# Optimization experiments

Hardware: AMD Instinct MI355X
Metric: run time of the kernel (lower is better)

The kernel has to match this reference:

```python
import jax, jax.numpy as jnp
import numpy as np

N = 26000       # total nodes (1040 graphs * 25 joints)
E = 208000      # total edges
G = 1040        # graphs (16 samples * 65 frames)
FRAMES = 65
F_IN = 6
HID = 128
HEADS = 4
NCLS = 7


def setup_inputs() -> dict:
    key = jax.random.key(0)
    ks = jax.random.split(key, 30)

    def nrm(k, shape, s=0.05):
        return jax.random.normal(k, shape, dtype=jnp.float32) * s

    return {
        "x": jax.random.normal(ks[0], (N, F_IN), dtype=jnp.float32),
        "edge_index": jax.random.randint(ks[1], (2, E), 0, N, dtype=jnp.int32),
        "batch": jnp.arange(N, dtype=jnp.int32) // (N // G),  # 25 nodes per graph
        "w1_root": nrm(ks[2], (F_IN, HID)),
        "w1_nei": nrm(ks[3], (F_IN, HID)),
        "b1": nrm(ks[4], (HID,)),
        "wq": nrm(ks[5], (HID, HEADS * HID)),
        "bq": nrm(ks[6], (HEADS * HID,)),
        "wk": nrm(ks[7], (HID, HEADS * HID)),
        "bk": nrm(ks[8], (HEADS * HID,)),
        "wv": nrm(ks[9], (HID, HEADS * HID)),
        "bv": nrm(ks[10], (HEADS * HID,)),
        "wskip": nrm(ks[11], (HID, HEADS * HID)),
        "bskip": nrm(ks[12], (HEADS * HID,)),
        "skip_w": nrm(ks[13], (HID, HEADS * HID)),
        "lin1_w": nrm(ks[14], (HEADS * HID, HID)),
        "lin1_b": nrm(ks[15], (HID,)),
        "l2_root": nrm(ks[16], (HID, HID)),
        "l2_nei": nrm(ks[17], (HID, HID)),
        "l2_b": nrm(ks[18], (HID,)),
        "l3_root": nrm(ks[19], (HID, HID)),
        "l3_nei": nrm(ks[20], (HID, HID)),
        "l3_b": nrm(ks[21], (HID,)),
        "fc_w": nrm(ks[22], (HID, NCLS)),
        "fc_b": nrm(ks[23], (NCLS,)),
    }


def _graph_conv(x, src, dst, w_root, w_nei, b):
    # PyG GraphConv (aggr='add'): W_root x_i + W_nei * sum_{j in N(i)} x_j + b
    agg = jax.ops.segment_sum(x[src], dst, num_segments=N)
    return x @ w_root + agg @ w_nei + b


def _transformer_conv(x, src, dst, wq, bq, wk, bk, wv, bv, wskip, bskip):
    # PyG TransformerConv, concat=True, root_weight=True, beta=False.
    # Dropout on attention is inference-disabled.
    q = (x @ wq + bq).reshape(N, HEADS, HID)
    k = (x @ wk + bk).reshape(N, HEADS, HID)
    v = (x @ wv + bv).reshape(N, HEADS, HID)
    logits = jnp.einsum('ehc,ehc->eh', q[dst], k[src]) / jnp.sqrt(jnp.float32(HID))
    m = jax.ops.segment_max(logits, dst, num_segments=N)          # [N,H]
    a = jnp.exp(logits - m[dst])                                  # [E,H]
    denom = jax.ops.segment_sum(a, dst, num_segments=N)           # [N,H]
    num = jax.ops.segment_sum(a[:, :, None] * v[src], dst, num_segments=N)  # [N,H,C]
    out = num / jnp.where(denom == 0, 1.0, denom)[:, :, None]
    return out.reshape(N, HEADS * HID) + (x @ wskip + bskip)


def reference(x, edge_index, batch,
              w1_root, w1_nei, b1,
              wq, bq, wk, bk, wv, bv, wskip, bskip,
              skip_w, lin1_w, lin1_b,
              l2_root, l2_nei, l2_b,
              l3_root, l3_nei, l3_b,
              fc_w, fc_b):
    src, dst = edge_index[0], edge_index[1]
    h = jax.nn.relu(_graph_conv(x, src, dst, w1_root, w1_nei, b1))
    skip_out = h @ skip_w  # external skip Linear (no bias)
    h = jax.nn.relu(_transformer_conv(h, src, dst, wq, bq, wk, bk, wv, bv, wskip, bskip) + skip_out)
    h = jax.nn.relu(h @ lin1_w + lin1_b)
    for wr, wn, b in ((l2_root, l2_nei, l2_b), (l3_root, l3_nei, l3_b)):
        h = jax.nn.relu(_graph_conv(h, src, dst, wr, wn, b) + h)
    # global_mean_pool over graphs
    sums = jax.ops.segment_sum(h, batch, num_segments=G)
    cnts = jax.ops.segment_sum(jnp.ones((N,), jnp.float32), batch, num_segments=G)
    pooled = sums / jnp.where(cnts == 0, 1.0, cnts)[:, None]      # [G, HID]
    # average over 65 frames per sample, then classify
    z = pooled.reshape(-1, FRAMES, HID).mean(axis=1)              # [G/65, HID]
    return z @ fc_w + fc_b
```

## Files before the change

kernel.cpp:

```cpp
#include <hip/hip_runtime.h>
#include <math.h>

#define NN 26000
#define NE 208000
#define SCAN_CH 26

typedef __attribute__((ext_vector_type(8))) short bf16x8;
typedef __attribute__((ext_vector_type(4))) float f32x4;
typedef __attribute__((ext_vector_type(2))) float f32x2;
typedef unsigned char u8;

__device__ __forceinline__ float bf2f(ushort u){
  union { unsigned int i; float f; } w; w.i = ((unsigned int)u) << 16; return w.f;
}
__device__ __forceinline__ ushort f2bf(float f){
  union { float f; unsigned int i; } w; w.f = f;
  unsigned int u = w.i + 0x7fffu + ((w.i >> 16) & 1u);
  return (ushort)(u >> 16);
}

__global__ void count_k(const int* __restrict__ dst, int* __restrict__ cnt, int E){
  int e = blockIdx.x*256 + threadIdx.x;
  if (e < E) atomicAdd(&cnt[dst[e]], 1);
}

__global__ __launch_bounds__(1024) void scan_k(int* __restrict__ cnt_cur, int* __restrict__ off){
  int t = threadIdx.x;
  int base = t * SCAN_CH;
  int v[SCAN_CH];
  #pragma unroll
  for (int j = 0; j < SCAN_CH; ++j){
    int idx = base + j;
    v[j] = (idx < NN) ? cnt_cur[idx] : 0;
  }
  int s = 0;
  #pragma unroll
  for (int j = 0; j < SCAN_CH; ++j) s += v[j];
  __shared__ int ls[1024];
  ls[t] = s; __syncthreads();
  for (int ofs = 1; ofs < 1024; ofs <<= 1){
    int u = (t >= ofs) ? ls[t - ofs] : 0;
    __syncthreads();
    ls[t] += u;
    __syncthreads();
  }
  int run = (t == 0) ? 0 : ls[t-1];
  #pragma unroll
  for (int j = 0; j < SCAN_CH; ++j){
    int idx = base + j;
    if (idx < NN){
      off[idx] = run;
      cnt_cur[idx] = run;
      run += v[j];
    }
  }
  if (t == 1023) off[NN] = ls[1023];
}

__global__ void fill_k(const int* __restrict__ src, const int* __restrict__ dst,
                       int* __restrict__ cur, int* __restrict__ csrc, int E){
  int e = blockIdx.x*256 + threadIdx.x;
  if (e < E){
    int p = atomicAdd(&cur[dst[e]], 1);
    csrc[p] = src[e];
  }
}

__global__ __launch_bounds__(256) void layer1_k(
    const float* __restrict__ x, const int* __restrict__ off,
    const int* __restrict__ csrc, const float* __restrict__ w1r,
    const float* __restrict__ w1n, const float* __restrict__ b1,
    ushort* __restrict__ h1)
{
  __shared__ float aggs[2][6];
  int slot = threadIdx.x >> 7, c = threadIdx.x & 127;
  int i = blockIdx.x*2 + slot;
  if (c < 6){
    float s = 0.f;
    int e1 = off[i+1];
    for (int j = off[i]; j < e1; ++j) s += x[(size_t)csrc[j]*6 + c];
    aggs[slot][c] = s;
  }
  __syncthreads();
  float s = b1[c];
  #pragma unroll
  for (int f = 0; f < 6; ++f){
    s = fmaf(x[i*6+f],    w1r[f*128+c], s);
    s = fmaf(aggs[slot][f], w1n[f*128+c], s);
  }
  h1[(size_t)i*128 + c] = f2bf(fmaxf(s, 0.f));
}

__global__ void prep_w(const float* __restrict__ wq, const float* __restrict__ wk,
                       const float* __restrict__ wv, const float* __restrict__ wskip,
                       const float* __restrict__ skw, const float* __restrict__ lin1w,
                       const float* __restrict__ l2r, const float* __restrict__ l2n,
                       const float* __restrict__ l3r, const float* __restrict__ l3n,
                       ushort* __restrict__ wbuf){
  int idx = blockIdx.x*256 + threadIdx.x;
  if (idx >= 393216) return;
  float v;
  if (idx < 262144){
    int seg = idx >> 16;
    int local = idx & 65535;
    int n = local >> 7, kk = local & 127;
    const float* w = (seg == 0) ? wq : (seg == 1) ? wk : (seg == 2) ? wv : wskip;
    v = w[kk*512 + n];
    if (seg == 3) v += skw[kk*512 + n];
  } else if (idx < 327680){
    int local = idx - 262144;
    int n = local >> 9, kk = local & 511;
    v = lin1w[kk*128 + n];
  } else {
    int rem = idx - 327680;
    int seg = rem >> 14;
    int local = rem & 16383;
    int n = local >> 7, kk = local & 127;
    const float* w = (seg == 0) ? l2r : (seg == 1) ? l2n : (seg == 2) ? l3r : l3n;
    v = w[kk*128 + n];
  }
  wbuf[idx] = f2bf(v);
}

__global__ __launch_bounds__(256) void qkvs_k(
    const ushort* __restrict__ A, const ushort* __restrict__ BT,
    const float* __restrict__ bq, const float* __restrict__ bk,
    const float* __restrict__ bv, const float* __restrict__ bs,
    u8* __restrict__ cq, u8* __restrict__ ckv,
    ushort* __restrict__ cs, int M)
{
  __shared__ ushort As[128][72];
  int tid  = threadIdx.x;
  int lane = tid & 63;
  int wid  = tid >> 6;
  int wr = wid >> 1, wc = wid & 1;
  int rowbase = blockIdx.y * 128;
  int seg = blockIdx.x >> 2;
  const float* bias = (seg == 0) ? bq : (seg == 1) ? bk : (seg == 2) ? bv : bs;
  int colloc = (blockIdx.x & 3) * 128;
  int lr = lane & 15, lk = (lane >> 4) * 8;

  f32x4 acc[4][4] = {};

  #pragma unroll
  for (int k0 = 0; k0 < 128; k0 += 64){
    __syncthreads();
    #pragma unroll
    for (int i = 0; i < 4; ++i){
      int c = tid + i*256;
      int r = c >> 3, col8 = (c & 7) * 8;
      int row = rowbase + r;
      bf16x8 av = (bf16x8)0;
      if (row < M) av = *reinterpret_cast<const bf16x8*>(A + (size_t)row*128 + k0 + col8);
      *reinterpret_cast<bf16x8*>(&As[r][col8]) = av;
    }
    __syncthreads();
    #pragma unroll
    for (int ks = 0; ks < 64; ks += 32){
      bf16x8 af[4], bfr[4];
      #pragma unroll
      for (int i = 0; i < 4; ++i)
        af[i] = *reinterpret_cast<const bf16x8*>(&As[wr*64 + i*16 + lr][ks + lk]);
      #pragma unroll
      for (int j = 0; j < 4; ++j)
        bfr[j] = *reinterpret_cast<const bf16x8*>(
            BT + (size_t)(blockIdx.x*128 + wc*64 + j*16 + lr)*128 + k0 + ks + lk);
      #pragma unroll
      for (int i = 0; i < 4; ++i)
        #pragma unroll
        for (int j = 0; j < 4; ++j)
          acc[i][j] = __builtin_amdgcn_mfma_f32_16x16x32_bf16(af[i], bfr[j], acc[i][j], 0, 0, 0);
    }
  }

  int rq = lane >> 4;
  if (seg <= 2){
    u8* tile = (u8*)&As[0][0];
    __syncthreads();
    #pragma unroll
    for (int i = 0; i < 4; ++i)
      #pragma unroll
      for (int r = 0; r < 4; ++r){
        int lrow = wr*64 + i*16 + rq*4 + r;
        #pragma unroll
        for (int j = 0; j < 4; ++j){
          int lcol = wc*64 + j*16 + lr;
          float v = acc[i][j][r] + bias[colloc + lcol];
          unsigned int pk = __builtin_amdgcn_cvt_pk_fp8_f32(v, v, 0u, false);
          tile[lrow*136 + lcol] = (u8)(pk & 0xffu);
        }
      }
    __syncthreads();
    u8* Cb; int ldb, cb;
    if (seg == 0){ Cb = cq;  ldb = 512;  cb = colloc; }
    else         { Cb = ckv; ldb = 1024; cb = (seg == 1 ? 0 : 512) + colloc; }
    #pragma unroll
    for (int t = tid; t < 2048; t += 256){
      int r = t >> 4, b8 = (t & 15) * 8;
      int row = rowbase + r;
      if (row < M)
        *reinterpret_cast<uint2*>(Cb + (size_t)row*ldb + cb + b8) =
            *reinterpret_cast<const uint2*>(&tile[r*136 + b8]);
    }
  } else {
    ushort* tile = &As[0][0];
    #pragma unroll
    for (int p = 0; p < 2; ++p){
      __syncthreads();
      if (wr == p){
        #pragma unroll
        for (int i = 0; i < 4; ++i)
          #pragma unroll
          for (int r = 0; r < 4; ++r){
            int lrow = i*16 + rq*4 + r;
            #pragma unroll
            for (int j = 0; j < 4; ++j){
              int lcol = wc*64 + j*16 + lr;
              tile[lrow*136 + lcol] = f2bf(acc[i][j][r] + bias[colloc + lcol]);
            }
          }
      }
      __syncthreads();
      #pragma unroll
      for (int t = tid; t < 1024; t += 256){
        int r = t >> 4, s8 = (t & 15) * 8;
        int row = rowbase + p*64 + r;
        if (row < M)
          *reinterpret_cast<bf16x8*>(cs + (size_t)row*512 + colloc + s8) =
              *reinterpret_cast<const bf16x8*>(&tile[r*136 + s8]);
      }
    }
  }
}

__global__ __launch_bounds__(256) void bgemm64_k(
    const ushort* __restrict__ A1, int lda1, const ushort* __restrict__ B1T, int K1,
    const float* __restrict__ bias, ushort* __restrict__ C, int M, int N)
{
  __shared__ ushort As[64][72];
  int tid  = threadIdx.x;
  int lane = tid & 63;
  int wid  = tid >> 6;
  int wr = wid >> 1, wc = wid & 1;
  int rowbase = blockIdx.y * 64;
  int colbase = blockIdx.x * 128;
  int lr = lane & 15, lk = (lane >> 4) * 8;

  f32x4 acc[2][4] = {};

  for (int k0 = 0; k0 < K1; k0 += 64){
    __syncthreads();
    #pragma unroll
    for (int i = 0; i < 2; ++i){
      int c = tid + i*256;
      int r = c >> 3, col8 = (c & 7) * 8;
      int row = rowbase + r;
      bf16x8 av = (bf16x8)0;
      if (row < M) av = *reinterpret_cast<const bf16x8*>(A1 + (size_t)row*lda1 + k0 + col8);
      *reinterpret_cast<bf16x8*>(&As[r][col8]) = av;
    }
    __syncthreads();
    #pragma unroll
    for (int ks = 0; ks < 64; ks += 32){
      bf16x8 af[2], bfr[4];
      #pragma unroll
      for (int i = 0; i < 2; ++i)
        af[i] = *reinterpret_cast<const bf16x8*>(&As[wr*32 + i*16 + lr][ks + lk]);
      #pragma unroll
      for (int j = 0; j < 4; ++j)
        bfr[j] = *reinterpret_cast<const bf16x8*>(
            B1T + (size_t)(colbase + wc*64 + j*16 + lr)*K1 + k0 + ks + lk);
      #pragma unroll
      for (int i = 0; i < 2; ++i)
        #pragma unroll
        for (int j = 0; j < 4; ++j)
          acc[i][j] = __builtin_amdgcn_mfma_f32_16x16x32_bf16(af[i], bfr[j], acc[i][j], 0, 0, 0);
    }
  }

  int rq = lane >> 4;
  #pragma unroll
  for (int i = 0; i < 2; ++i){
    #pragma unroll
    for (int r = 0; r < 4; ++r){
      int row = rowbase + wr*32 + i*16 + rq*4 + r;
      if (row >= M) continue;
      #pragma unroll
      for (int j = 0; j < 4; ++j){
        int col = colbase + wc*64 + j*16 + lr;
        if (col >= N) continue;
        float v = fmaxf(acc[i][j][r] + bias[col], 0.f);
        C[(size_t)row*N + col] = f2bf(v);
      }
    }
  }
}

__global__ __launch_bounds__(256) void gconv_k(
    const ushort* __restrict__ h, const ushort* __restrict__ WrT,
    const ushort* __restrict__ WnT, const float* __restrict__ bias,
    const int* __restrict__ off, const int* __restrict__ csrc,
    ushort* __restrict__ out, int M)
{
  __shared__ ushort As1[64][136];
  __shared__ ushort As2[64][136];
  int tid = threadIdx.x, lane = tid & 63, wid = tid >> 6;
  int wr = wid >> 1, wc = wid & 1;
  int rowbase = blockIdx.x * 64;
  int lr = lane & 15, lk = (lane >> 4) * 8;

  #pragma unroll
  for (int it = 0; it < 4; ++it){
    int c = tid + it*256;
    int r = c >> 4, col8 = (c & 15) * 8;
    int row = rowbase + r;
    bf16x8 av = (bf16x8)0;
    if (row < M) av = *reinterpret_cast<const bf16x8*>(h + (size_t)row*128 + col8);
    *reinterpret_cast<bf16x8*>(&As1[r][col8]) = av;
  }
  {
    int r = tid >> 2, sl = tid & 3;
    int row = rowbase + r;
    float a[32] = {};
    if (row < M){
      int e1 = off[row+1];
      for (int j = off[row]; j < e1; ++j){
        const ushort* hp = h + (size_t)csrc[j]*128 + sl*32;
        #pragma unroll
        for (int u = 0; u < 4; ++u){
          bf16x8 hv = *reinterpret_cast<const bf16x8*>(hp + u*8);
          #pragma unroll
          for (int p = 0; p < 8; ++p) a[u*8+p] += bf2f((ushort)hv[p]);
        }
      }
    }
    #pragma unroll
    for (int u = 0; u < 4; ++u){
      bf16x8 o;
      #pragma unroll
      for (int p = 0; p < 8; ++p) o[p] = (short)f2bf(a[u*8+p]);
      *reinterpret_cast<bf16x8*>(&As2[r][sl*32 + u*8]) = o;
    }
  }
  __syncthreads();

  f32x4 acc[2][4] = {};
  #pragma unroll
  for (int pass = 0; pass < 2; ++pass){
    const ushort* BT = pass ? WnT : WrT;
    #pragma unroll
    for (int kk = 0; kk < 128; kk += 32){
      bf16x8 af[2], bfr[4];
      #pragma unroll
      for (int i = 0; i < 2; ++i)
        af[i] = pass
          ? *reinterpret_cast<const bf16x8*>(&As2[wr*32 + i*16 + lr][kk + lk])
          : *reinterpret_cast<const bf16x8*>(&As1[wr*32 + i*16 + lr][kk + lk]);
      #pragma unroll
      for (int j = 0; j < 4; ++j)
        bfr[j] = *reinterpret_cast<const bf16x8*>(
            BT + (size_t)(wc*64 + j*16 + lr)*128 + kk + lk);
      #pragma unroll
      for (int i = 0; i < 2; ++i)
        #pragma unroll
        for (int j = 0; j < 4; ++j)
          acc[i][j] = __builtin_amdgcn_mfma_f32_16x16x32_bf16(af[i], bfr[j], acc[i][j], 0, 0, 0);
    }
  }

  int rq = lane >> 4;
  #pragma unroll
  for (int i = 0; i < 2; ++i){
    #pragma unroll
    for (int r = 0; r < 4; ++r){
      int lrow = wr*32 + i*16 + rq*4 + r;
      int row = rowbase + lrow;
      if (row >= M) continue;
      #pragma unroll
      for (int j = 0; j < 4; ++j){
        int col = wc*64 + j*16 + lr;
        float v = acc[i][j][r] + bias[col] + bf2f(As1[lrow][col]);
        out[(size_t)row*128 + col] = f2bf(fmaxf(v, 0.f));
      }
    }
  }
}

__global__ __launch_bounds__(256) void attn_k(
    const u8* __restrict__ q, const u8* __restrict__ kv,
    ushort* __restrict__ s_io,
    const int* __restrict__ off, const int* __restrict__ csrc)
{
  int lane = threadIdx.x & 63;
  int i = blockIdx.x*4 + (threadIdx.x >> 6);
  uint2 qv = *reinterpret_cast<const uint2*>(q + (size_t)i*512 + lane*8);
  f32x2 q01 = __builtin_amdgcn_cvt_pk_f32_fp8(qv.x, false);
  f32x2 q23 = __builtin_amdgcn_cvt_pk_f32_fp8(qv.x, true);
  f32x2 q45 = __builtin_amdgcn_cvt_pk_f32_fp8(qv.y, false);
  f32x2 q67 = __builtin_amdgcn_cvt_pk_f32_fp8(qv.y, true);
  float qf[8] = {q01[0], q01[1], q23[0], q23[1], q45[0], q45[1], q67[0], q67[1]};

  float d = 0.f, acc[8] = {};
  int e0 = off[i], e1 = off[i+1];
  uint2 kA, vA, kB, vB;
  if (e0 < e1){
    const u8* r = kv + (size_t)csrc[e0]*1024 + lane*8;
    kA = *reinterpret_cast<const uint2*>(r);
    vA = *reinterpret_cast<const uint2*>(r + 512);
  }
  if (e0 + 1 < e1){
    const u8* r = kv + (size_t)csrc[e0+1]*1024 + lane*8;
    kB = *reinterpret_cast<const uint2*>(r);
    vB = *reinterpret_cast<const uint2*>(r + 512);
  }
  for (int j = e0; j < e1; ++j){
    uint2 kc = kA, vc = vA;
    kA = kB; vA = vB;
    if (j + 2 < e1){
      const u8* r = kv + (size_t)csrc[j+2]*1024 + lane*8;
      kB = *reinterpret_cast<const uint2*>(r);
      vB = *reinterpret_cast<const uint2*>(r + 512);
    }
    f32x2 k01 = __builtin_amdgcn_cvt_pk_f32_fp8(kc.x, false);
    f32x2 k23 = __builtin_amdgcn_cvt_pk_f32_fp8(kc.x, true);
    f32x2 k45 = __builtin_amdgcn_cvt_pk_f32_fp8(kc.y, false);
    f32x2 k67 = __builtin_amdgcn_cvt_pk_f32_fp8(kc.y, true);
    float t;
    t = qf[0] * k01[0];
    t = fmaf(qf[1], k01[1], t);
    t = fmaf(qf[2], k23[0], t);
    t = fmaf(qf[3], k23[1], t);
    t = fmaf(qf[4], k45[0], t);
    t = fmaf(qf[5], k45[1], t);
    t = fmaf(qf[6], k67[0], t);
    t = fmaf(qf[7], k67[1], t);
    t += __shfl_xor(t, 1);
    t += __shfl_xor(t, 2);
    t += __shfl_xor(t, 4);
    t += __shfl_xor(t, 8);
    float w = __expf(t * 0.08838834764831845f);
    d += w;
    f32x2 v01 = __builtin_amdgcn_cvt_pk_f32_fp8(vc.x, false);
    f32x2 v23 = __builtin_amdgcn_cvt_pk_f32_fp8(vc.x, true);
    f32x2 v45 = __builtin_amdgcn_cvt_pk_f32_fp8(vc.y, false);
    f32x2 v67 = __builtin_amdgcn_cvt_pk_f32_fp8(vc.y, true);
    acc[0] = fmaf(w, v01[0], acc[0]);
    acc[1] = fmaf(w, v01[1], acc[1]);
    acc[2] = fmaf(w, v23[0], acc[2]);
    acc[3] = fmaf(w, v23[1], acc[3]);
    acc[4] = fmaf(w, v45[0], acc[4]);
    acc[5] = fmaf(w, v45[1], acc[5]);
    acc[6] = fmaf(w, v67[0], acc[6]);
    acc[7] = fmaf(w, v67[1], acc[7]);
  }
  float inv = (d > 0.f) ? 1.f/d : 0.f;
  ushort* rowp = s_io + (size_t)i*512 + lane*8;
  bf16x8 sk8 = *reinterpret_cast<const bf16x8*>(rowp);
  bf16x8 o8;
  #pragma unroll
  for (int p = 0; p < 8; ++p)
    o8[p] = (short)f2bf(fmaxf(bf2f((ushort)sk8[p]) + acc[p]*inv, 0.f));
  *reinterpret_cast<bf16x8*>(rowp) = o8;
}

__global__ __launch_bounds__(256) void fc1_k(const ushort* __restrict__ h,
                                             float* __restrict__ partial){
  int s = blockIdx.x, c0 = blockIdx.y;
  int t = threadIdx.x;
  int c = t & 127, g = t >> 7;
  float sum = 0.f;
  int rend = (c0 + 1) * 125;
  for (int r = c0*125 + g; r < rend; r += 2)
    sum += bf2f(h[((size_t)s*1625 + r)*128 + c]);
  __shared__ float zs[2][128];
  zs[g][c] = sum; __syncthreads();
  if (g == 0) partial[((size_t)s*13 + c0)*128 + c] = zs[0][c] + zs[1][c];
}

__global__ __launch_bounds__(128) void fc2_k(const float* __restrict__ partial,
    const float* __restrict__ fcw, const float* __restrict__ fcb,
    float* __restrict__ out)
{
  int s = blockIdx.x;
  int c = threadIdx.x;
  float z = 0.f;
  #pragma unroll
  for (int p = 0; p < 13; ++p) z += partial[((size_t)s*13 + p)*128 + c];
  __shared__ float zs[128];
  zs[c] = z * (1.0f/1625.0f);
  __syncthreads();
  if (c < 7){
    float o = fcb[c];
    for (int k2 = 0; k2 < 128; ++k2) o = fmaf(zs[k2], fcw[k2*7 + c], o);
    out[s*7 + c] = o;
  }
}

extern "C" void kernel_launch(void* const* d_in, const int* in_sizes, int n_in,
                              void* d_out, int out_size, void* d_ws, size_t ws_size,
                              hipStream_t stream)
{
  const float* x     = (const float*)d_in[0];
  const int*   ei    = (const int*)  d_in[1];
  const float* w1r   = (const float*)d_in[3];
  const float* w1n   = (const float*)d_in[4];
  const float* b1    = (const float*)d_in[5];
  const float* wq    = (const float*)d_in[6];
  const float* bq    = (const float*)d_in[7];
  const float* wk    = (const float*)d_in[8];
  const float* bk    = (const float*)d_in[9];
  const float* wv    = (const float*)d_in[10];
  const float* bv    = (const float*)d_in[11];
  const float* wskip = (const float*)d_in[12];
  const float* bskip = (const float*)d_in[13];
  const float* skw   = (const float*)d_in[14];
  const float* lin1w = (const float*)d_in[15];
  const float* lin1b = (const float*)d_in[16];
  const float* l2r   = (const float*)d_in[17];
  const float* l2n   = (const float*)d_in[18];
  const float* l2b   = (const float*)d_in[19];
  const float* l3r   = (const float*)d_in[20];
  const float* l3n   = (const float*)d_in[21];
  const float* l3b   = (const float*)d_in[22];
  const float* fcw   = (const float*)d_in[23];
  const float* fcb   = (const float*)d_in[24];
  float* out = (float*)d_out;

  const int* src = ei;
  const int* dst = ei + NE;

  char* base = (char*)d_ws;
  size_t o = 0;
  auto alloc = [&](size_t bytes) -> void* {
    o = (o + 255) & ~(size_t)255;
    void* p = base + o; o += bytes; return p;
  };
  int*    cnt     = (int*)   alloc((size_t)NN*4);
  int*    off     = (int*)   alloc((size_t)(NN+1)*4);
  int*    csrc    = (int*)   alloc((size_t)NE*4);
  float*  partial = (float*) alloc((size_t)16*13*128*4);
  ushort* h1      = (ushort*)alloc((size_t)NN*128*2);
  ushort* wbuf    = (ushort*)alloc((size_t)393216*2);
  u8*     bufQ8   = (u8*)    alloc((size_t)NN*512);
  u8*     bufKV   = (u8*)    alloc((size_t)NN*1024);
  ushort* bufS    = (ushort*)alloc((size_t)NN*512*2);
  ushort* hbuf    = (ushort*)alloc((size_t)NN*256*2);
  (void)ws_size; (void)in_sizes; (void)n_in; (void)out_size;

  const ushort* lin1T = wbuf + 262144;
  const ushort* l2rT  = wbuf + 327680;
  const ushort* l2nT  = wbuf + 344064;
  const ushort* l3rT  = wbuf + 360448;
  const ushort* l3nT  = wbuf + 376832;

  ushort* h3 = hbuf;
  ushort* h4 = hbuf + (size_t)NN*128;
  ushort* h5 = bufS;

  hipMemsetAsync(cnt, 0, (size_t)NN*4, stream);
  count_k<<<(NE+255)/256, 256, 0, stream>>>(dst, cnt, NE);
  scan_k<<<1, 1024, 0, stream>>>(cnt, off);
  fill_k<<<(NE+255)/256, 256, 0, stream>>>(src, dst, cnt, csrc, NE);

  layer1_k<<<NN/2, 256, 0, stream>>>(x, off, csrc, w1r, w1n, b1, h1);

  prep_w<<<1536, 256, 0, stream>>>(wq, wk, wv, wskip, skw, lin1w, l2r, l2n, l3r, l3n, wbuf);

  {
    dim3 g(16, (NN+127)/128);
    qkvs_k<<<g, 256, 0, stream>>>(h1, wbuf, bq, bk, bv, bskip,
                                  bufQ8, bufKV, bufS, NN);
  }

  attn_k<<<NN/4, 256, 0, stream>>>(bufQ8, bufKV, bufS, off, csrc);

  {
    dim3 g(1, (NN+63)/64);
    bgemm64_k<<<g, 256, 0, stream>>>(bufS, 512, lin1T, 512, lin1b, h3, NN, 128);
  }

  gconv_k<<<(NN+63)/64, 256, 0, stream>>>(h3, l2rT, l2nT, l2b, off, csrc, h4, NN);
  gconv_k<<<(NN+63)/64, 256, 0, stream>>>(h4, l3rT, l3nT, l3b, off, csrc, h5, NN);

  {
    dim3 g1(16, 13);
    fc1_k<<<g1, 256, 0, stream>>>(h5, partial);
    fc2_k<<<16, 128, 0, stream>>>(partial, fcw, fcb, out);
  }
}
```

Before: 304.6 us.

## Fuse edge count with weight prep, stage B tiles in LDS, merge final FC kernels

Merges the degree-count kernel and the weight-conversion kernel into one launch by splitting blocks by index. The QKVS and bgemm GEMMs now stage the B (weight) tile in shared memory instead of reading it straight from global per fragment. The QKVS epilogue writes bf16 to LDS once and converts to fp8 with packed 4-wide conversions. The two-stage pooling/classifier becomes a single kernel with 16 blocks. That removes launches, but the per-sample reduction of 1625 rows now runs on very few blocks.

```diff
diff --git a/kernel.cpp b/kernel.cpp
--- a/kernel.cpp
+++ b/kernel.cpp
@@ -4,6 +4,7 @@
 #define NN 26000
 #define NE 208000
 #define SCAN_CH 26
+#define CNT_BLOCKS 813
 
 typedef __attribute__((ext_vector_type(8))) short bf16x8;
 typedef __attribute__((ext_vector_type(4))) float f32x4;
@@ -19,85 +20,19 @@
   return (ushort)(u >> 16);
 }
 
-__global__ void count_k(const int* __restrict__ dst, int* __restrict__ cnt, int E){
-  int e = blockIdx.x*256 + threadIdx.x;
-  if (e < E) atomicAdd(&cnt[dst[e]], 1);
-}
-
-__global__ __launch_bounds__(1024) void scan_k(int* __restrict__ cnt_cur, int* __restrict__ off){
-  int t = threadIdx.x;
-  int base = t * SCAN_CH;
-  int v[SCAN_CH];
-  #pragma unroll
-  for (int j = 0; j < SCAN_CH; ++j){
-    int idx = base + j;
-    v[j] = (idx < NN) ? cnt_cur[idx] : 0;
-  }
-  int s = 0;
-  #pragma unroll
-  for (int j = 0; j < SCAN_CH; ++j) s += v[j];
-  __shared__ int ls[1024];
-  ls[t] = s; __syncthreads();
-  for (int ofs = 1; ofs < 1024; ofs <<= 1){
-    int u = (t >= ofs) ? ls[t - ofs] : 0;
-    __syncthreads();
-    ls[t] += u;
-    __syncthreads();
-  }
-  int run = (t == 0) ? 0 : ls[t-1];
-  #pragma unroll
-  for (int j = 0; j < SCAN_CH; ++j){
-    int idx = base + j;
-    if (idx < NN){
-      off[idx] = run;
-      cnt_cur[idx] = run;
-      run += v[j];
-    }
-  }
-  if (t == 1023) off[NN] = ls[1023];
-}
-
-__global__ void fill_k(const int* __restrict__ src, const int* __restrict__ dst,
-                       int* __restrict__ cur, int* __restrict__ csrc, int E){
-  int e = blockIdx.x*256 + threadIdx.x;
-  if (e < E){
-    int p = atomicAdd(&cur[dst[e]], 1);
-    csrc[p] = src[e];
-  }
-}
-
-__global__ __launch_bounds__(256) void layer1_k(
-    const float* __restrict__ x, const int* __restrict__ off,
-    const int* __restrict__ csrc, const float* __restrict__ w1r,
-    const float* __restrict__ w1n, const float* __restrict__ b1,
-    ushort* __restrict__ h1)
-{
-  __shared__ float aggs[2][6];
-  int slot = threadIdx.x >> 7, c = threadIdx.x & 127;
-  int i = blockIdx.x*2 + slot;
-  if (c < 6){
-    float s = 0.f;
-    int e1 = off[i+1];
-    for (int j = off[i]; j < e1; ++j) s += x[(size_t)csrc[j]*6 + c];
-    aggs[slot][c] = s;
-  }
-  __syncthreads();
-  float s = b1[c];
-  #pragma unroll
-  for (int f = 0; f < 6; ++f){
-    s = fmaf(x[i*6+f],    w1r[f*128+c], s);
-    s = fmaf(aggs[slot][f], w1n[f*128+c], s);
-  }
-  h1[(size_t)i*128 + c] = f2bf(fmaxf(s, 0.f));
-}
-
-__global__ void prep_w(const float* __restrict__ wq, const float* __restrict__ wk,
-                       const float* __restrict__ wv, const float* __restrict__ wskip,
-                       const float* __restrict__ skw, const float* __restrict__ lin1w,
-                       const float* __restrict__ l2r, const float* __restrict__ l2n,
-                       const float* __restrict__ l3r, const float* __restrict__ l3n,
-                       ushort* __restrict__ wbuf){
-  int idx = blockIdx.x*256 + threadIdx.x;
+__global__ void cp_k(const int* __restrict__ dst, int* __restrict__ cnt,
+                     const float* __restrict__ wq, const float* __restrict__ wk,
+                     const float* __restrict__ wv, const float* __restrict__ wskip,
+                     const float* __restrict__ skw, const float* __restrict__ lin1w,
+                     const float* __restrict__ l2r, const float* __restrict__ l2n,
+                     const float* __restrict__ l3r, const float* __restrict__ l3n,
+                     ushort* __restrict__ wbuf){
+  if (blockIdx.x < CNT_BLOCKS){
+    int e = blockIdx.x*256 + threadIdx.x;
+    if (e < NE) atomicAdd(&cnt[dst[e]], 1);
+    return;
+  }
+  int idx = (blockIdx.x - CNT_BLOCKS)*256 + threadIdx.x;
   if (idx >= 393216) return;
   float v;
   if (idx < 262144){
@@ -122,6 +57,73 @@
   wbuf[idx] = f2bf(v);
 }
 
+__global__ __launch_bounds__(1024) void scan_k(int* __restrict__ cnt_cur, int* __restrict__ off){
+  int t = threadIdx.x;
+  int base = t * SCAN_CH;
+  int v[SCAN_CH];
+  #pragma unroll
+  for (int j = 0; j < SCAN_CH; ++j){
+    int idx = base + j;
+    v[j] = (idx < NN) ? cnt_cur[idx] : 0;
+  }
+  int s = 0;
+  #pragma unroll
+  for (int j = 0; j < SCAN_CH; ++j) s += v[j];
+  __shared__ int ls[1024];
+  ls[t] = s; __syncthreads();
+  for (int ofs = 1; ofs < 1024; ofs <<= 1){
+    int u = (t >= ofs) ? ls[t - ofs] : 0;
+    __syncthreads();
+    ls[t] += u;
+    __syncthreads();
+  }
+  int run = (t == 0) ? 0 : ls[t-1];
+  #pragma unroll
+  for (int j = 0; j < SCAN_CH; ++j){
+    int idx = base + j;
+    if (idx < NN){
+      off[idx] = run;
+      cnt_cur[idx] = run;
+      run += v[j];
+    }
+  }
+  if (t == 1023) off[NN] = ls[1023];
+}
+
+__global__ void fill_k(const int* __restrict__ src, const int* __restrict__ dst,
+                       int* __restrict__ cur, int* __restrict__ csrc, int E){
+  int e = blockIdx.x*256 + threadIdx.x;
+  if (e < E){
+    int p = atomicAdd(&cur[dst[e]], 1);
+    csrc[p] = src[e];
+  }
+}
+
+__global__ __launch_bounds__(256) void layer1_k(
+    const float* __restrict__ x, const int* __restrict__ off,
+    const int* __restrict__ csrc, const float* __restrict__ w1r,
+    const float* __restrict__ w1n, const float* __restrict__ b1,
+    ushort* __restrict__ h1)
+{
+  __shared__ float aggs[2][6];
+  int slot = threadIdx.x >> 7, c = threadIdx.x & 127;
+  int i = blockIdx.x*2 + slot;
+  if (c < 6){
+    float s = 0.f;
+    int e1 = off[i+1];
+    for (int j = off[i]; j < e1; ++j) s += x[(size_t)csrc[j]*6 + c];
+    aggs[slot][c] = s;
+  }
+  __syncthreads();
+  float s = b1[c];
+  #pragma unroll
+  for (int f = 0; f < 6; ++f){
+    s = fmaf(x[i*6+f],    w1r[f*128+c], s);
+    s = fmaf(aggs[slot][f], w1n[f*128+c], s);
+  }
+  h1[(size_t)i*128 + c] = f2bf(fmaxf(s, 0.f));
+}
+
 __global__ __launch_bounds__(256) void qkvs_k(
     const ushort* __restrict__ A, const ushort* __restrict__ BT,
     const float* __restrict__ bq, const float* __restrict__ bk,
@@ -129,7 +131,9 @@
     u8* __restrict__ cq, u8* __restrict__ ckv,
     ushort* __restrict__ cs, int M)
 {
-  __shared__ ushort As[128][72];
+  __shared__ ushort smem[2*128*72];
+  ushort* Asm = smem;
+  ushort* Bsm = smem + 128*72;
   int tid  = threadIdx.x;
   int lane = tid & 63;
   int wid  = tid >> 6;
@@ -142,9 +146,7 @@
 
   f32x4 acc[4][4] = {};
 
-  #pragma unroll
   for (int k0 = 0; k0 < 128; k0 += 64){
-    __syncthreads();
     #pragma unroll
     for (int i = 0; i < 4; ++i){
       int c = tid + i*256;
@@ -152,7 +154,9 @@
       int row = rowbase + r;
       bf16x8 av = (bf16x8)0;
       if (row < M) av = *reinterpret_cast<const bf16x8*>(A + (size_t)row*128 + k0 + col8);
-      *reinterpret_cast<bf16x8*>(&As[r][col8]) = av;
+      *reinterpret_cast<bf16x8*>(&Asm[r*72 + col8]) = av;
+      *reinterpret_cast<bf16x8*>(&Bsm[r*72 + col8]) =
+          *reinterpret_cast<const bf16x8*>(BT + (size_t)(blockIdx.x*128 + r)*128 + k0 + col8);
     }
     __syncthreads();
     #pragma unroll
@@ -160,75 +164,60 @@
       bf16x8 af[4], bfr[4];
       #pragma unroll
       for (int i = 0; i < 4; ++i)
-        af[i] = *reinterpret_cast<const bf16x8*>(&As[wr*64 + i*16 + lr][ks + lk]);
+        af[i] = *reinterpret_cast<const bf16x8*>(&Asm[(wr*64 + i*16 + lr)*72 + ks + lk]);
       #pragma unroll
       for (int j = 0; j < 4; ++j)
-        bfr[j] = *reinterpret_cast<const bf16x8*>(
-            BT + (size_t)(blockIdx.x*128 + wc*64 + j*16 + lr)*128 + k0 + ks + lk);
+        bfr[j] = *reinterpret_cast<const bf16x8*>(&Bsm[(wc*64 + j*16 + lr)*72 + ks + lk]);
       #pragma unroll
       for (int i = 0; i < 4; ++i)
         #pragma unroll
         for (int j = 0; j < 4; ++j)
           acc[i][j] = __builtin_amdgcn_mfma_f32_16x16x32_bf16(af[i], bfr[j], acc[i][j], 0, 0, 0);
     }
+    __syncthreads();
   }
 
   int rq = lane >> 4;
+  #pragma unroll
+  for (int i = 0; i < 4; ++i)
+    #pragma unroll
+    for (int r = 0; r < 4; ++r){
+      int lrow = wr*64 + i*16 + rq*4 + r;
+      #pragma unroll
+      for (int j = 0; j < 4; ++j){
+        int lcol = wc*64 + j*16 + lr;
+        smem[lrow*136 + lcol] = f2bf(acc[i][j][r] + bias[colloc + lcol]);
+      }
+    }
+  __syncthreads();
+
   if (seg <= 2){
-    u8* tile = (u8*)&As[0][0];
-    __syncthreads();
-    #pragma unroll
-    for (int i = 0; i < 4; ++i)
-      #pragma unroll
-      for (int r = 0; r < 4; ++r){
-        int lrow = wr*64 + i*16 + rq*4 + r;
-        #pragma unroll
-        for (int j = 0; j < 4; ++j){
-          int lcol = wc*64 + j*16 + lr;
-          float v = acc[i][j][r] + bias[colloc + lcol];
-          unsigned int pk = __builtin_amdgcn_cvt_pk_fp8_f32(v, v, 0u, false);
-          tile[lrow*136 + lcol] = (u8)(pk & 0xffu);
-        }
-      }
-    __syncthreads();
     u8* Cb; int ldb, cb;
     if (seg == 0){ Cb = cq;  ldb = 512;  cb = colloc; }
     else         { Cb = ckv; ldb = 1024; cb = (seg == 1 ? 0 : 512) + colloc; }
     #pragma unroll
     for (int t = tid; t < 2048; t += 256){
-      int r = t >> 4, b8 = (t & 15) * 8;
+      int r = t >> 4, s8 = (t & 15) * 8;
+      int row = rowbase + r;
+      if (row < M){
+        bf16x8 hv = *reinterpret_cast<const bf16x8*>(&smem[r*136 + s8]);
+        unsigned int lo = 0, hi = 0;
+        lo = __builtin_amdgcn_cvt_pk_fp8_f32(bf2f((ushort)hv[0]), bf2f((ushort)hv[1]), lo, false);
+        lo = __builtin_amdgcn_cvt_pk_fp8_f32(bf2f((ushort)hv[2]), bf2f((ushort)hv[3]), lo, true);
+        hi = __builtin_amdgcn_cvt_pk_fp8_f32(bf2f((ushort)hv[4]), bf2f((ushort)hv[5]), hi, false);
+        hi = __builtin_amdgcn_cvt_pk_fp8_f32(bf2f((ushort)hv[6]), bf2f((ushort)hv[7]), hi, true);
+        uint2 o; o.x = lo; o.y = hi;
+        *reinterpret_cast<uint2*>(Cb + (size_t)row*ldb + cb + s8) = o;
+      }
+    }
+  } else {
+    #pragma unroll
+    for (int t = tid; t < 2048; t += 256){
+      int r = t >> 4, s8 = (t & 15) * 8;
       int row = rowbase + r;
       if (row < M)
-        *reinterpret_cast<uint2*>(Cb + (size_t)row*ldb + cb + b8) =
-            *reinterpret_cast<const uint2*>(&tile[r*136 + b8]);
-    }
-  } else {
-    ushort* tile = &As[0][0];
-    #pragma unroll
-    for (int p = 0; p < 2; ++p){
-      __syncthreads();
-      if (wr == p){
-        #pragma unroll
-        for (int i = 0; i < 4; ++i)
-          #pragma unroll
-          for (int r = 0; r < 4; ++r){
-            int lrow = i*16 + rq*4 + r;
-            #pragma unroll
-            for (int j = 0; j < 4; ++j){
-              int lcol = wc*64 + j*16 + lr;
-              tile[lrow*136 + lcol] = f2bf(acc[i][j][r] + bias[colloc + lcol]);
-            }
-          }
-      }
-      __syncthreads();
-      #pragma unroll
-      for (int t = tid; t < 1024; t += 256){
-        int r = t >> 4, s8 = (t & 15) * 8;
-        int row = rowbase + p*64 + r;
-        if (row < M)
-          *reinterpret_cast<bf16x8*>(cs + (size_t)row*512 + colloc + s8) =
-              *reinterpret_cast<const bf16x8*>(&tile[r*136 + s8]);
-      }
+        *reinterpret_cast<bf16x8*>(cs + (size_t)row*512 + colloc + s8) =
+            *reinterpret_cast<const bf16x8*>(&smem[r*136 + s8]);
     }
   }
 }
@@ -238,6 +227,7 @@
     const float* __restrict__ bias, ushort* __restrict__ C, int M, int N)
 {
   __shared__ ushort As[64][72];
+  __shared__ ushort Bs[128][72];
   int tid  = threadIdx.x;
   int lane = tid & 63;
   int wid  = tid >> 6;
@@ -249,7 +239,6 @@
   f32x4 acc[2][4] = {};
 
   for (int k0 = 0; k0 < K1; k0 += 64){
-    __syncthreads();
     #pragma unroll
     for (int i = 0; i < 2; ++i){
       int c = tid + i*256;
@@ -259,6 +248,13 @@
       if (row < M) av = *reinterpret_cast<const bf16x8*>(A1 + (size_t)row*lda1 + k0 + col8);
       *reinterpret_cast<bf16x8*>(&As[r][col8]) = av;
     }
+    #pragma unroll
+    for (int i = 0; i < 4; ++i){
+      int c = tid + i*256;
+      int r = c >> 3, col8 = (c & 7) * 8;
+      *reinterpret_cast<bf16x8*>(&Bs[r][col8]) =
+          *reinterpret_cast<const bf16x8*>(B1T + (size_t)(colbase + r)*K1 + k0 + col8);
+    }
     __syncthreads();
     #pragma unroll
     for (int ks = 0; ks < 64; ks += 32){
@@ -268,14 +264,14 @@
         af[i] = *reinterpret_cast<const bf16x8*>(&As[wr*32 + i*16 + lr][ks + lk]);
       #pragma unroll
       for (int j = 0; j < 4; ++j)
-        bfr[j] = *reinterpret_cast<const bf16x8*>(
-            B1T + (size_t)(colbase + wc*64 + j*16 + lr)*K1 + k0 + ks + lk);
+        bfr[j] = *reinterpret_cast<const bf16x8*>(&Bs[wc*64 + j*16 + lr][ks + lk]);
       #pragma unroll
       for (int i = 0; i < 2; ++i)
         #pragma unroll
         for (int j = 0; j < 4; ++j)
           acc[i][j] = __builtin_amdgcn_mfma_f32_16x16x32_bf16(af[i], bfr[j], acc[i][j], 0, 0, 0);
     }
+    __syncthreads();
   }
 
   int rq = lane >> 4;
@@ -463,36 +459,24 @@
   *reinterpret_cast<bf16x8*>(rowp) = o8;
 }
 
-__global__ __launch_bounds__(256) void fc1_k(const ushort* __restrict__ h,
-                                             float* __restrict__ partial){
-  int s = blockIdx.x, c0 = blockIdx.y;
+__global__ __launch_bounds__(256) void fc_k(const ushort* __restrict__ h,
+    const float* __restrict__ fcw, const float* __restrict__ fcb,
+    float* __restrict__ out)
+{
+  int s = blockIdx.x;
   int t = threadIdx.x;
   int c = t & 127, g = t >> 7;
   float sum = 0.f;
-  int rend = (c0 + 1) * 125;
-  for (int r = c0*125 + g; r < rend; r += 2)
+  for (int r = g; r < 1625; r += 2)
     sum += bf2f(h[((size_t)s*1625 + r)*128 + c]);
   __shared__ float zs[2][128];
   zs[g][c] = sum; __syncthreads();
-  if (g == 0) partial[((size_t)s*13 + c0)*128 + c] = zs[0][c] + zs[1][c];
-}
-
-__global__ __launch_bounds__(128) void fc2_k(const float* __restrict__ partial,
-    const float* __restrict__ fcw, const float* __restrict__ fcb,
-    float* __restrict__ out)
-{
-  int s = blockIdx.x;
-  int c = threadIdx.x;
-  float z = 0.f;
-  #pragma unroll
-  for (int p = 0; p < 13; ++p) z += partial[((size_t)s*13 + p)*128 + c];
-  __shared__ float zs[128];
-  zs[c] = z * (1.0f/1625.0f);
+  if (t < 128) zs[0][t] = (zs[0][t] + zs[1][t]) * (1.0f/1625.0f);
   __syncthreads();
-  if (c < 7){
-    float o = fcb[c];
-    for (int k2 = 0; k2 < 128; ++k2) o = fmaf(zs[k2], fcw[k2*7 + c], o);
-    out[s*7 + c] = o;
+  if (t < 7){
+    float o = fcb[t];
+    for (int k2 = 0; k2 < 128; ++k2) o = fmaf(zs[0][k2], fcw[k2*7 + t], o);
+    out[s*7 + t] = o;
   }
 }
 
@@ -538,7 +522,6 @@
   int*    cnt     = (int*)   alloc((size_t)NN*4);
   int*    off     = (int*)   alloc((size_t)(NN+1)*4);
   int*    csrc    = (int*)   alloc((size_t)NE*4);
-  float*  partial = (float*) alloc((size_t)16*13*128*4);
   ushort* h1      = (ushort*)alloc((size_t)NN*128*2);
   ushort* wbuf    = (ushort*)alloc((size_t)393216*2);
   u8*     bufQ8   = (u8*)    alloc((size_t)NN*512);
@@ -558,13 +541,12 @@
   ushort* h5 = bufS;
 
   hipMemsetAsync(cnt, 0, (size_t)NN*4, stream);
-  count_k<<<(NE+255)/256, 256, 0, stream>>>(dst, cnt, NE);
+  cp_k<<<CNT_BLOCKS + 1536, 256, 0, stream>>>(dst, cnt,
+      wq, wk, wv, wskip, skw, lin1w, l2r, l2n, l3r, l3n, wbuf);
   scan_k<<<1, 1024, 0, stream>>>(cnt, off);
   fill_k<<<(NE+255)/256, 256, 0, stream>>>(src, dst, cnt, csrc, NE);
 
   layer1_k<<<NN/2, 256, 0, stream>>>(x, off, csrc, w1r, w1n, b1, h1);
-
-  prep_w<<<1536, 256, 0, stream>>>(wq, wk, wv, wskip, skw, lin1w, l2r, l2n, l3r, l3n, wbuf);
 
   {
     dim3 g(16, (NN+127)/128);
@@ -582,9 +564,5 @@
   gconv_k<<<(NN+63)/64, 256, 0, stream>>>(h3, l2rT, l2nT, l2b, off, csrc, h4, NN);
   gconv_k<<<(NN+63)/64, 256, 0, stream>>>(h4, l3rT, l3nT, l3b, off, csrc, h5, NN);
 
-  {
-    dim3 g1(16, 13);
-    fc1_k<<<g1, 256, 0, stream>>>(h5, partial);
-    fc2_k<<<16, 128, 0, stream>>>(partial, fcw, fcb, out);
-  }
-}
+  fc_k<<<16, 256, 0, stream>>>(h5, fcw, fcb, out);
+}
```

After: 460.4 us. 1.51x slower.
